# Kernel optimization log

Hardware: AMD Instinct MI355X
Metric: run time of the kernel (lower is better)

Reference implementation:

```python
import jax, jax.numpy as jnp
import numpy as np

C = jnp.complex64

# Hadamard gate
_HG = jnp.asarray(np.array([[1.0, 1.0], [1.0, -1.0]]) / np.sqrt(2.0), dtype=C)


def _rx(angles):
    # angles: [P] -> batched RX gates [P, 2, 2]
    c = jnp.cos(angles / 2).astype(C)
    s = (-1j * jnp.sin(angles / 2)).astype(C)
    return jnp.stack([jnp.stack([c, s], -1), jnp.stack([s, c], -1)], -2)


def _x_theta(theta):
    # X_theta_gate with cos(pi/2)=0, sin(pi/2)=1:
    # [[0, -i e^{i t/2}], [-i e^{-i t/2}, 0]]
    e = jnp.exp(0.5j * theta.astype(C))
    z = jnp.zeros((), C)
    row0 = jnp.stack([z, -1j * e])
    row1 = jnp.stack([-1j * jnp.conj(e), z])
    return jnp.stack([row0, row1])


def _cu(theta):
    # controlled-U as rank-4 tensor CU[c_out, t_out, c_in, t_in]
    cu = jnp.zeros((2, 2, 2, 2), C)
    cu = cu.at[0, :, 0, :].set(jnp.eye(2, dtype=C))
    cu = cu.at[1, :, 1, :].set(_x_theta(theta))
    return cu

# state axes: p (patch), a..e = wires 0..4
_RX_SPECS = ['pij,pajcde->paicde', 'pij,pabjde->pabide',
             'pij,pabcje->pabcie', 'pij,pabcdj->pabcdi']
# controlled gates: (ctrl1,tgt2), (ctrl2,tgt3), (ctrl3,tgt4), (ctrl4,tgt1)
_CU_SPECS = ['ijkl,paklde->paijde', 'ijkl,pabkle->pabije',
             'ijkl,pabckl->pabcij', 'ijkl,palcdk->pajcdi']


def _simulate(pix, thetas, phis):
    # pix: [P, 12] per-patch angles; returns <Z_0> per patch, [P]
    P = pix.shape[0]
    s = jnp.zeros((P, 2, 2, 2, 2, 2), C).at[:, 0, 0, 0, 0, 0].set(1.0)
    s = jnp.einsum('ij,pjbcde->pibcde', _HG, s)  # H on wire 0
    for layer in range(3):
        for w in range(4):
            g = _rx(pix[:, 4 * layer + w])
            s = jnp.einsum(_RX_SPECS[w], g, s)
        for w in range(4):
            cu = _cu(thetas[4 * layer + w])
            s = jnp.einsum(_CU_SPECS[w], cu, s)
        # CPhase(phi) on wires [0, 1]
        phase = jnp.ones((2, 2), C).at[1, 1].set(jnp.exp(1j * phis[layer].astype(C)))
        s = s * phase[None, :, :, None, None, None]
    s = jnp.einsum('ij,pjbcde->pibcde', _HG, s)  # final H on wire 0
    sign = jnp.array([1.0, -1.0], jnp.float32)
    probs = jnp.abs(s) ** 2
    return jnp.sum(probs * sign[None, :, None, None, None, None], axis=(1, 2, 3, 4, 5))


def setup_inputs() -> dict:
    key = jax.random.key(0)
    k1, k2, k3 = jax.random.split(key, 3)
    x = jax.random.normal(k1, (16, 3, 256, 256), dtype=jnp.float32)
    thetas = jax.random.normal(k2, (12,), dtype=jnp.float32)
    phis = jax.random.normal(k3, (3,), dtype=jnp.float32)
    return {'x': x, 'thetas': thetas, 'phis': phis}


def reference(x, thetas, phis):
    B, Cch, H, W = x.shape
    H2, W2 = H // 2, W // 2
    # extract 2x2 patches: order per patch = [(0,0),(0,1),(1,0),(1,1)] per channel
    pix = x.reshape(B, 3, H2, 2, W2, 2).transpose(0, 2, 4, 1, 3, 5).reshape(B * H2 * W2, 12)
    ev = _simulate(pix, thetas, phis)  # [P]
    return ev.reshape(B, 1, H2, W2).astype(jnp.float32)
```

## Files before the change

### kernel.cpp

```cpp
#include <hip/hip_runtime.h>


typedef float f2 __attribute__((ext_vector_type(2)));

__device__ __forceinline__ void sc_half(float ang, float& s, float& c) {
    const float r = ang * 0.07957747154594767f;
    s = __builtin_amdgcn_sinf(r);
    c = __builtin_amdgcn_cosf(r);
}
__device__ __forceinline__ void sc_full(float ang, float& s, float& c) {
    const float r = ang * 0.15915494309189535f;
    s = __builtin_amdgcn_sinf(r);
    c = __builtin_amdgcn_cosf(r);
}

template<int BIT>
__device__ __forceinline__ void apply_rx(f2 (&R)[16], f2 (&I)[16],
                                         float c, float s) {
#pragma unroll
    for (int m = 0; m < 8; ++m) {
        const int lo = m & ((1 << BIT) - 1);
        const int hi = (m >> BIT) << (BIT + 1);
        const int i0 = hi | lo;
        const int i1 = i0 | (1 << BIT);
        const f2 ar = R[i0], ai = I[i0];
        const f2 br = R[i1], bi = I[i1];
        R[i0] = c * ar + s * bi;
        I[i0] = c * ai - s * br;
        R[i1] = c * br + s * ai;
        I[i1] = c * bi - s * ar;
    }
}

template<int CBIT, int TBIT>
__device__ __forceinline__ void cu_gate(f2 (&R)[16], f2 (&I)[16],
                                        float sn, float cs) {
#pragma unroll
    for (int m = 0; m < 8; ++m) {
        const int lo = m & ((1 << TBIT) - 1);
        const int hi = (m >> TBIT) << (TBIT + 1);
        const int i0 = hi | lo;
        if (!(i0 & (1 << CBIT))) continue;
        const int i1 = i0 | (1 << TBIT);
        const f2 ar = R[i0], ai = I[i0];
        const f2 br = R[i1], bi = I[i1];
        R[i0] =  sn * br + cs * bi;
        I[i0] =  sn * bi - cs * br;
        R[i1] = -sn * ar + cs * ai;
        I[i1] = -sn * ai - cs * ar;
    }
}

__device__ __forceinline__ void cphase(f2 (&R)[16], f2 (&I)[16],
                                       float sn, float cs) {
    const f2 C = {1.f, cs}, S = {0.f, sn};
#pragma unroll
    for (int m = 8; m < 16; ++m) {
        const f2 r = R[m], ii = I[m];
        R[m] = C * r  - S * ii;
        I[m] = C * ii + S * r;
    }
}

__global__ __launch_bounds__(256, 4)
void qsim_kernel(const float* __restrict__ x,
                 const float* __restrict__ thetas,
                 const float* __restrict__ phis,
                 float* __restrict__ out, int P) {
    const int p = blockIdx.x * blockDim.x + threadIdx.x;
    if (p >= P) return;

    const int b   = p >> 14;
    const int rem = p & 16383;
    const int i   = rem >> 7;
    const int j   = rem & 127;

    const float2* __restrict__ x2 = (const float2*)x;
    const long rowbase = (long)b * 768 + 2 * i;

    float2 v0 = x2[(rowbase + 0) * 128 + j];
    float2 v1 = x2[(rowbase + 1) * 128 + j];

    f2 R[16], I[16];
    {
        float s1, c1, s2, c2, s3, c3, s4, c4;
        sc_half(v0.x, s1, c1);
        sc_half(v0.y, s2, c2);
        sc_half(v1.x, s3, c3);
        sc_half(v1.y, s4, c4);
        const float pA[4] = {c1 * c2, c1 * s2, s1 * c2, s1 * s2};
        const float pB[4] = {c3 * c4, c3 * s4, s3 * c4, s3 * s4};
#pragma unroll
        for (int m = 0; m < 16; ++m) {
            const float v = pA[m >> 2] * pB[m & 3];
            const int pc = __builtin_popcount((unsigned)m) & 3;
            const float rr = (pc == 0) ? v : ((pc == 2) ? -v : 0.f);
            const float ii = (pc == 1) ? -v : ((pc == 3) ? v : 0.f);
            R[m] = (f2){rr, rr};
            I[m] = (f2){ii, ii};
        }
    }

    v0 = x2[(rowbase + 256) * 128 + j];
    v1 = x2[(rowbase + 257) * 128 + j];

    {
        float sn, cs;
        sc_half(thetas[0], sn, cs); cu_gate<3, 2>(R, I, sn, cs);
        sc_half(thetas[1], sn, cs); cu_gate<2, 1>(R, I, sn, cs);
        sc_half(thetas[2], sn, cs); cu_gate<1, 0>(R, I, sn, cs);
        sc_half(thetas[3], sn, cs); cu_gate<0, 3>(R, I, sn, cs);
    }
    {
        float sn, cs;
        sc_full(phis[0], sn, cs);
        cphase(R, I, sn, cs);
    }

    {
        float sn, cs;
        sc_half(v0.x, sn, cs); apply_rx<3>(R, I, cs, sn);
        sc_half(v0.y, sn, cs); apply_rx<2>(R, I, cs, sn);
        sc_half(v1.x, sn, cs); apply_rx<1>(R, I, cs, sn);
        sc_half(v1.y, sn, cs); apply_rx<0>(R, I, cs, sn);
    }
    v0 = x2[(rowbase + 512) * 128 + j];
    v1 = x2[(rowbase + 513) * 128 + j];

    {
        float sn, cs;
        sc_half(thetas[4], sn, cs); cu_gate<3, 2>(R, I, sn, cs);
        sc_half(thetas[5], sn, cs); cu_gate<2, 1>(R, I, sn, cs);
        sc_half(thetas[6], sn, cs); cu_gate<1, 0>(R, I, sn, cs);
        sc_half(thetas[7], sn, cs); cu_gate<0, 3>(R, I, sn, cs);
    }
    {
        float sn, cs;
        sc_full(phis[1], sn, cs);
        cphase(R, I, sn, cs);
    }

    {
        float sn, cs;
        sc_half(v0.x, sn, cs); apply_rx<3>(R, I, cs, sn);
        sc_half(v0.y, sn, cs); apply_rx<2>(R, I, cs, sn);
        sc_half(v1.x, sn, cs); apply_rx<1>(R, I, cs, sn);
        sc_half(v1.y, sn, cs); apply_rx<0>(R, I, cs, sn);
    }
    {
        float sn, cs;
        sc_half(thetas[ 8], sn, cs); cu_gate<3, 2>(R, I, sn, cs);
        sc_half(thetas[ 9], sn, cs); cu_gate<2, 1>(R, I, sn, cs);
        sc_half(thetas[10], sn, cs); cu_gate<1, 0>(R, I, sn, cs);
        sc_half(thetas[11], sn, cs); cu_gate<0, 3>(R, I, sn, cs);
    }
    {
        float sn, cs;
        sc_full(phis[2], sn, cs);
        cphase(R, I, sn, cs);
    }

    float ev = 0.f;
#pragma unroll
    for (int m = 0; m < 16; ++m) {
        ev += R[m].x * R[m].y + I[m].x * I[m].y;
    }
    out[p] = ev;
}

extern "C" void kernel_launch(void* const* d_in, const int* in_sizes, int n_in,
                              void* d_out, int out_size, void* d_ws, size_t ws_size,
                              hipStream_t stream) {
    const float* x      = (const float*)d_in[0];
    const float* thetas = (const float*)d_in[1];
    const float* phis   = (const float*)d_in[2];
    float* out = (float*)d_out;
    const int P = out_size;
    const int threads = 256;
    const int blocks = (P + threads - 1) / threads;
    qsim_kernel<<<blocks, threads, 0, stream>>>(x, thetas, phis, out, P);
}
```

Measured before the change: 71.84 us.

## Fold CU chain and CPhase into precomputed diagonal-permutation and analytic final layer

Each layer's four controlled X_theta gates plus the CPhase form a monomial matrix, a permutation times a diagonal. A tiny prologue kernel now precomputes the diagonal phases per layer into workspace, and the main kernel applies them as one elementwise complex multiply with a compile-time register permutation. The last layer's entangling block is folded into the expectation value analytically, using a parity-split sum and a cos/sin correction. This removes most of the per-thread gate arithmetic and transcendentals. The cost is an extra kernel launch and 32 float4 loads per thread from global memory, which should mostly hit cache. The occupancy hint in launch_bounds is also dropped.

```diff
diff --git a/kernel.cpp b/kernel.cpp
--- a/kernel.cpp
+++ b/kernel.cpp
@@ -12,6 +12,12 @@
     const float r = ang * 0.15915494309189535f;
     s = __builtin_amdgcn_sinf(r);
     c = __builtin_amdgcn_cosf(r);
+}
+
+__host__ __device__ constexpr int PI_(int m) {
+    const int m3 = (m >> 3) & 1, m2 = (m >> 2) & 1, m1 = (m >> 1) & 1, m0 = m & 1;
+    return ((m0 ^ m1 ^ m2) << 3) | ((m2 ^ m3) << 2) |
+           ((m1 ^ m2 ^ m3) << 1) | (m0 ^ m1 ^ m2 ^ m3);
 }
 
 template<int BIT>
@@ -32,39 +38,42 @@
     }
 }
 
-template<int CBIT, int TBIT>
-__device__ __forceinline__ void cu_gate(f2 (&R)[16], f2 (&I)[16],
-                                        float sn, float cs) {
+__global__ void diag_kernel(const float* __restrict__ thetas,
+                            const float* __restrict__ phis,
+                            float* __restrict__ g) {
+    const int tid = threadIdx.x;
+    if (tid >= 32) return;
+    const int L = tid >> 4, m = tid & 15;
+    float ar[4], ai[4], br[4], bi[4];
 #pragma unroll
-    for (int m = 0; m < 8; ++m) {
-        const int lo = m & ((1 << TBIT) - 1);
-        const int hi = (m >> TBIT) << (TBIT + 1);
-        const int i0 = hi | lo;
-        if (!(i0 & (1 << CBIT))) continue;
-        const int i1 = i0 | (1 << TBIT);
-        const f2 ar = R[i0], ai = I[i0];
-        const f2 br = R[i1], bi = I[i1];
-        R[i0] =  sn * br + cs * bi;
-        I[i0] =  sn * bi - cs * br;
-        R[i1] = -sn * ar + cs * ai;
-        I[i1] = -sn * ai - cs * ar;
+    for (int k = 0; k < 4; ++k) {
+        float sn, cs; sc_half(thetas[4 * L + k], sn, cs);
+        ar[k] = sn;  ai[k] = -cs;
+        br[k] = -sn; bi[k] = -cs;
     }
+    const int m3 = (m >> 3) & 1, m2 = (m >> 2) & 1, m1 = (m >> 1) & 1, m0 = m & 1;
+    float cr = 1.f, ci = 0.f;
+#define MULC(xr, xi) { const float nr = cr*(xr) - ci*(xi); \
+                       const float ni = cr*(xi) + ci*(xr); cr = nr; ci = ni; }
+    if (m3)            { if (m2) MULC(ar[0], ai[0]) else MULC(br[0], bi[0]) }
+    const int t2 = m2 ^ m3;
+    if (t2)            { if (m1) MULC(ar[1], ai[1]) else MULC(br[1], bi[1]) }
+    const int t1 = m1 ^ t2;
+    if (t1)            { if (m0) MULC(ar[2], ai[2]) else MULC(br[2], bi[2]) }
+    const int t0 = m0 ^ t1;
+    if (t0)            { if (m3) MULC(ar[3], ai[3]) else MULC(br[3], bi[3]) }
+#undef MULC
+    const int cond = m3 ^ t0;
+    float sp_, cp_; sc_full(phis[L], sp_, cp_);
+    float cyr = cr, cyi = ci;
+    if (cond) { cyr = cr * cp_ - ci * sp_; cyi = cr * sp_ + ci * cp_; }
+    float4 o; o.x = cr; o.y = cyr; o.z = ci; o.w = cyi;
+    reinterpret_cast<float4*>(g)[L * 16 + m] = o;
 }
 
-__device__ __forceinline__ void cphase(f2 (&R)[16], f2 (&I)[16],
-                                       float sn, float cs) {
-    const f2 C = {1.f, cs}, S = {0.f, sn};
-#pragma unroll
-    for (int m = 8; m < 16; ++m) {
-        const f2 r = R[m], ii = I[m];
-        R[m] = C * r  - S * ii;
-        I[m] = C * ii + S * r;
-    }
-}
-
-__global__ __launch_bounds__(256, 4)
+__global__ __launch_bounds__(256)
 void qsim_kernel(const float* __restrict__ x,
-                 const float* __restrict__ thetas,
+                 const float* __restrict__ g,
                  const float* __restrict__ phis,
                  float* __restrict__ out, int P) {
     const int p = blockIdx.x * blockDim.x + threadIdx.x;
@@ -104,66 +113,62 @@
     v0 = x2[(rowbase + 256) * 128 + j];
     v1 = x2[(rowbase + 257) * 128 + j];
 
-    {
-        float sn, cs;
-        sc_half(thetas[0], sn, cs); cu_gate<3, 2>(R, I, sn, cs);
-        sc_half(thetas[1], sn, cs); cu_gate<2, 1>(R, I, sn, cs);
-        sc_half(thetas[2], sn, cs); cu_gate<1, 0>(R, I, sn, cs);
-        sc_half(thetas[3], sn, cs); cu_gate<0, 3>(R, I, sn, cs);
-    }
-    {
-        float sn, cs;
-        sc_full(phis[0], sn, cs);
-        cphase(R, I, sn, cs);
+    const float4* __restrict__ g4 = (const float4*)g;
+
+    f2 Ra[16], Ia[16];
+#pragma unroll
+    for (int m = 0; m < 16; ++m) {
+        const float4 t = g4[m];
+        const f2 gr = {t.x, t.y}, gi = {t.z, t.w};
+        const f2 r = R[m], ii = I[m];
+        Ra[PI_(m)] = gr * r  - gi * ii;
+        Ia[PI_(m)] = gr * ii + gi * r;
     }
 
     {
         float sn, cs;
-        sc_half(v0.x, sn, cs); apply_rx<3>(R, I, cs, sn);
-        sc_half(v0.y, sn, cs); apply_rx<2>(R, I, cs, sn);
-        sc_half(v1.x, sn, cs); apply_rx<1>(R, I, cs, sn);
-        sc_half(v1.y, sn, cs); apply_rx<0>(R, I, cs, sn);
+        sc_half(v0.x, sn, cs); apply_rx<3>(Ra, Ia, cs, sn);
+        sc_half(v0.y, sn, cs); apply_rx<2>(Ra, Ia, cs, sn);
+        sc_half(v1.x, sn, cs); apply_rx<1>(Ra, Ia, cs, sn);
+        sc_half(v1.y, sn, cs); apply_rx<0>(Ra, Ia, cs, sn);
     }
     v0 = x2[(rowbase + 512) * 128 + j];
     v1 = x2[(rowbase + 513) * 128 + j];
 
-    {
-        float sn, cs;
-        sc_half(thetas[4], sn, cs); cu_gate<3, 2>(R, I, sn, cs);
-        sc_half(thetas[5], sn, cs); cu_gate<2, 1>(R, I, sn, cs);
-        sc_half(thetas[6], sn, cs); cu_gate<1, 0>(R, I, sn, cs);
-        sc_half(thetas[7], sn, cs); cu_gate<0, 3>(R, I, sn, cs);
-    }
-    {
-        float sn, cs;
-        sc_full(phis[1], sn, cs);
-        cphase(R, I, sn, cs);
+    f2 Rb[16], Ib[16];
+#pragma unroll
+    for (int m = 0; m < 16; ++m) {
+        const float4 t = g4[16 + m];
+        const f2 gr = {t.x, t.y}, gi = {t.z, t.w};
+        const f2 r = Ra[m], ii = Ia[m];
+        Rb[PI_(m)] = gr * r  - gi * ii;
+        Ib[PI_(m)] = gr * ii + gi * r;
     }
 
     {
         float sn, cs;
-        sc_half(v0.x, sn, cs); apply_rx<3>(R, I, cs, sn);
-        sc_half(v0.y, sn, cs); apply_rx<2>(R, I, cs, sn);
-        sc_half(v1.x, sn, cs); apply_rx<1>(R, I, cs, sn);
-        sc_half(v1.y, sn, cs); apply_rx<0>(R, I, cs, sn);
+        sc_half(v0.x, sn, cs); apply_rx<3>(Rb, Ib, cs, sn);
+        sc_half(v0.y, sn, cs); apply_rx<2>(Rb, Ib, cs, sn);
+        sc_half(v1.x, sn, cs); apply_rx<1>(Rb, Ib, cs, sn);
+        sc_half(v1.y, sn, cs); apply_rx<0>(Rb, Ib, cs, sn);
+    }
+
+    float ev = 0.f, zr = 0.f, zi = 0.f;
+#pragma unroll
+    for (int m = 0; m < 16; ++m) {
+        const int cond = ((m >> 2) ^ (m >> 1) ^ m) & 1;
+        const f2 r = Rb[m], ii = Ib[m];
+        const float prr = r.x * r.y + ii.x * ii.y;
+        if (cond) {
+            zr += prr;
+            zi += ii.x * r.y - r.x * ii.y;
+        } else {
+            ev += prr;
+        }
     }
     {
-        float sn, cs;
-        sc_half(thetas[ 8], sn, cs); cu_gate<3, 2>(R, I, sn, cs);
-        sc_half(thetas[ 9], sn, cs); cu_gate<2, 1>(R, I, sn, cs);
-        sc_half(thetas[10], sn, cs); cu_gate<1, 0>(R, I, sn, cs);
-        sc_half(thetas[11], sn, cs); cu_gate<0, 3>(R, I, sn, cs);
-    }
-    {
-        float sn, cs;
-        sc_full(phis[2], sn, cs);
-        cphase(R, I, sn, cs);
-    }
-
-    float ev = 0.f;
-#pragma unroll
-    for (int m = 0; m < 16; ++m) {
-        ev += R[m].x * R[m].y + I[m].x * I[m].y;
+        float sn, cs; sc_full(phis[2], sn, cs);
+        ev += cs * zr + sn * zi;
     }
     out[p] = ev;
 }
@@ -175,8 +180,10 @@
     const float* thetas = (const float*)d_in[1];
     const float* phis   = (const float*)d_in[2];
     float* out = (float*)d_out;
+    float* g   = (float*)d_ws;
     const int P = out_size;
     const int threads = 256;
     const int blocks = (P + threads - 1) / threads;
-    qsim_kernel<<<blocks, threads, 0, stream>>>(x, thetas, phis, out, P);
+    diag_kernel<<<1, 64, 0, stream>>>(thetas, phis, g);
+    qsim_kernel<<<blocks, threads, 0, stream>>>(x, g, phis, out, P);
 }
```

New measurement: 71.68 us. Within noise of the previous version (-0.2%).
